# Kernel tuning notes

Hardware: AMD Instinct MI355X
Metric: run time of the kernel (lower is better)

## Reference

```python
import jax, jax.numpy as jnp
import numpy as np

OBS_X, OBS_Y, RADIUS = 40.0, 15.0, 6.0
B = 524288  # batch of states


def setup_inputs() -> dict:
    key = jax.random.key(0)
    ks = jax.random.split(key, 14)
    def lin_w(k, o, i):
        return jax.random.normal(k, (o, i), jnp.float32) * (1.0 / np.sqrt(i))
    return {
        "x": jax.random.normal(ks[0], (B, 5), jnp.float32),
        "sgn": 1,
        "mean": jax.random.normal(ks[1], (5,), jnp.float32),
        "std": jax.random.uniform(ks[2], (5,), jnp.float32, minval=0.5, maxval=1.5),
        "fc1_w": lin_w(ks[3], 128, 5),
        "fc1_b": jax.random.normal(ks[4], (128,), jnp.float32) * 0.1,
        "fc21_w": lin_w(ks[5], 32, 128),
        "fc21_b": jax.random.normal(ks[6], (32,), jnp.float32) * 0.1,
        "fc22_w": lin_w(ks[7], 32, 128),
        "fc22_b": jax.random.normal(ks[8], (32,), jnp.float32) * 0.1,
        "fc31_w": lin_w(ks[9], 2, 32),
        "fc31_b": jax.random.normal(ks[10], (2,), jnp.float32) * 0.1,
        "fc32_w": lin_w(ks[11], 2, 32),
        "fc32_b": jax.random.normal(ks[12], (2,), jnp.float32) * 0.1,
    }


def reference(x, sgn, mean, std, fc1_w, fc1_b, fc21_w, fc21_b,
              fc22_w, fc22_b, fc31_w, fc31_b, fc32_w, fc32_b):
    # --- tiny MLP (DynamicUnicycle2D config: 5 -> 128 -> {32,32} -> {2,2}) ---
    x0 = x * std + mean                                   # de-normalized state [B,5]
    h1 = jax.nn.relu(x @ fc1_w.T + fc1_b)                 # [B,128]
    x21 = jax.nn.relu(h1 @ fc21_w.T + fc21_b)             # [B,32]
    x22 = jax.nn.relu(h1 @ fc22_w.T + fc22_b)             # [B,32]
    x31 = x21 @ fc31_w.T + fc31_b                         # QP linear cost p, [B,2]
    x32 = 4.0 * jax.nn.sigmoid(x22 @ fc32_w.T + fc32_b)   # CBF class-K gains, [B,2]

    # --- CBF derivation (relative degree 2, circular obstacle) ---
    px, py, theta, v = x0[:, 0], x0[:, 1], x0[:, 2], x0[:, 3]
    s, c = jnp.sin(theta), jnp.cos(theta)
    dx, dy = px - OBS_X, py - OBS_Y
    barrier = dx * dx + dy * dy - RADIUS * RADIUS
    barrier_dot = 2.0 * dx * v * c + 2.0 * dy * v * s
    Lf2b = 2.0 * v * v
    LgLfbu1 = -2.0 * dx * v * s + 2.0 * dy * v * c
    LgLfbu2 = 2.0 * dx * c + 2.0 * dy * s
    G = jnp.stack([-LgLfbu1, -LgLfbu2], axis=1)           # [B,2], single row constraint
    h = Lf2b + (x32[:, 0] + x32[:, 1]) * barrier_dot + x32[:, 0] * x32[:, 1] * barrier  # [B]

    # --- batched QP: min 0.5 u^T u + p^T u  s.t.  G u <= h  (Q = I, one constraint)
    # Exact KKT solution: project unconstrained optimum onto the half-space.
    u0 = -x31                                             # unconstrained optimum
    viol = jnp.sum(G * u0, axis=1) - h                    # [B]
    gg = jnp.sum(G * G, axis=1)                           # [B]
    lam = jnp.maximum(viol, 0.0) / (gg + 1e-12)           # active-set multiplier
    u = u0 - lam[:, None] * G                             # [B,2] safe control
    return u
```

## Files before the change

kernel.cpp:

```cpp
#include <hip/hip_runtime.h>
#include <hip/hip_bf16.h>
#include <math.h>

typedef __attribute__((ext_vector_type(8))) _Float16 half8;
typedef __attribute__((ext_vector_type(4))) float f32x4;

#define OBS_X 40.0f
#define OBS_Y 15.0f
#define RADIUS 6.0f

__device__ __forceinline__ unsigned short f16hi(float v) {
    _Float16 h = (_Float16)v;
    return __builtin_bit_cast(unsigned short, h);
}
__device__ __forceinline__ float f16f(unsigned short b) {
    return (float)__builtin_bit_cast(_Float16, b);
}

__global__ void prep_kernel(const float* __restrict__ w1,
                            const float* __restrict__ w21,
                            const float* __restrict__ w22,
                            unsigned short* __restrict__ ws) {
    int tid = blockIdx.x * blockDim.x + threadIdx.x;
#pragma unroll
    for (int m = 0; m < 2; ++m) {
        int idx = tid * 2 + m;
        int j = idx & 7, l = (idx >> 3) & 63, kc = (idx >> 9) & 3, t = idx >> 11;
        int c = t * 16 + (l & 15);
        int k = kc * 32 + (l >> 4) * 8 + j;
        float v = (c < 32) ? w21[c * 128 + k] : w22[(c - 32) * 128 + k];
        _Float16 h  = (_Float16)v;
        _Float16 lo = (_Float16)(v - (float)h);
        ws[idx]        = __builtin_bit_cast(unsigned short, h);
        ws[8192 + idx] = __builtin_bit_cast(unsigned short, lo);
    }
    if (tid < 1024) {
        int j = tid & 7, fr = tid >> 3;
        float v = (j < 5) ? w1[fr * 5 + j] : 0.0f;
        _Float16 h  = (_Float16)v;
        _Float16 lo = (_Float16)(v - (float)h);
        ws[16384 + tid] = __builtin_bit_cast(unsigned short, h);
        ws[17408 + tid] = __builtin_bit_cast(unsigned short, lo);
    }
}

#define MFMA4(acc, ah_, al_, bh_, bl_)                                      \
    acc = __builtin_amdgcn_mfma_f32_16x16x32_f16(al_, bl_, acc, 0, 0, 0);   \
    acc = __builtin_amdgcn_mfma_f32_16x16x32_f16(al_, bh_, acc, 0, 0, 0);   \
    acc = __builtin_amdgcn_mfma_f32_16x16x32_f16(ah_, bl_, acc, 0, 0, 0);   \
    acc = __builtin_amdgcn_mfma_f32_16x16x32_f16(ah_, bh_, acc, 0, 0, 0);

__global__ __launch_bounds__(256, 4) void barriernet_mfma(
    const float* __restrict__ x,
    const float* __restrict__ mean_, const float* __restrict__ std_,
    const float* __restrict__ b1,
    const float* __restrict__ b21, const float* __restrict__ b22,
    const float* __restrict__ w31, const float* __restrict__ b31,
    const float* __restrict__ w32, const float* __restrict__ b32,
    const unsigned short* __restrict__ ws,
    float* __restrict__ out)
{
    __shared__ unsigned char smem[4 * 8192];
    const int tid  = threadIdx.x;
    const int lane = tid & 63;
    const int wv   = tid >> 6;
    const int r16  = lane & 15;
    const int g    = lane >> 4;
    unsigned char* h1hi = smem + wv * 8192;
    unsigned char* h1lo = h1hi + 4096;

    const int rowbase = blockIdx.x * 64 + wv * 16;
    const unsigned swz = ((unsigned)(r16 & 7)) << 4;

    float xv0 = 0.f, xv1 = 0.f, xv2 = 0.f, xv3 = 0.f;
    half8 bxh = {0,0,0,0,0,0,0,0}, bxl = {0,0,0,0,0,0,0,0};
    if (lane < 16) {
        const float* xr = x + (size_t)(rowbase + r16) * 5;
        float v4;
        xv0 = xr[0]; xv1 = xr[1]; xv2 = xr[2]; xv3 = xr[3]; v4 = xr[4];
        _Float16 h;
        h = (_Float16)xv0; bxh[0] = h; bxl[0] = (_Float16)(xv0 - (float)h);
        h = (_Float16)xv1; bxh[1] = h; bxl[1] = (_Float16)(xv1 - (float)h);
        h = (_Float16)xv2; bxh[2] = h; bxl[2] = (_Float16)(xv2 - (float)h);
        h = (_Float16)xv3; bxh[3] = h; bxl[3] = (_Float16)(xv3 - (float)h);
        h = (_Float16)v4;  bxh[4] = h; bxl[4] = (_Float16)(v4  - (float)h);
    }

#pragma unroll
    for (int t = 0; t < 8; ++t) {
        half8 awh = {0,0,0,0,0,0,0,0}, awl = {0,0,0,0,0,0,0,0};
        if (lane < 16) {
            awh = *(const half8*)(ws + 16384 + (t * 16 + lane) * 8);
            awl = *(const half8*)(ws + 17408 + (t * 16 + lane) * 8);
        }
        const float4 bb = *(const float4*)(b1 + t * 16 + g * 4);
        f32x4 acc = {bb.x, bb.y, bb.z, bb.w};
        MFMA4(acc, awh, awl, bxh, bxl);
        float v0 = fmaxf(acc[0], 0.f), v1 = fmaxf(acc[1], 0.f);
        float v2 = fmaxf(acc[2], 0.f), v3 = fmaxf(acc[3], 0.f);
        unsigned short h0 = f16hi(v0), h1v = f16hi(v1), h2 = f16hi(v2), h3 = f16hi(v3);
        unsigned short l0 = f16hi(v0 - f16f(h0)), l1 = f16hi(v1 - f16f(h1v));
        unsigned short l2 = f16hi(v2 - f16f(h2)), l3 = f16hi(v3 - f16f(h3));
        const unsigned off = ((unsigned)(32 * t + 8 * g)) ^ swz;
        uint2 ph; ph.x = (unsigned)h0 | ((unsigned)h1v << 16); ph.y = (unsigned)h2 | ((unsigned)h3 << 16);
        uint2 pl; pl.x = (unsigned)l0 | ((unsigned)l1  << 16); pl.y = (unsigned)l2 | ((unsigned)l3 << 16);
        *(uint2*)(h1hi + r16 * 256 + off) = ph;
        *(uint2*)(h1lo + r16 * 256 + off) = pl;
    }

    half8 ah[4], al[4];
#pragma unroll
    for (int kc = 0; kc < 4; ++kc) {
        const unsigned off = ((unsigned)(kc * 64 + g * 16)) ^ swz;
        ah[kc] = *(const half8*)(h1hi + r16 * 256 + off);
        al[kc] = *(const half8*)(h1lo + r16 * 256 + off);
    }
    f32x4 acc2[4];
#pragma unroll
    for (int t = 0; t < 4; ++t) {
        const float bias = (t < 2) ? b21[t * 16 + r16] : b22[(t - 2) * 16 + r16];
        f32x4 a = {bias, bias, bias, bias};
#pragma unroll
        for (int kc = 0; kc < 4; ++kc) {
            const half8 bh = *(const half8*)(ws + ((t * 4 + kc) * 64 + lane) * 8);
            const half8 bl = *(const half8*)(ws + 8192 + ((t * 4 + kc) * 64 + lane) * 8);
            MFMA4(a, ah[kc], al[kc], bh, bl);
        }
        acc2[t] = a;
    }

    const float w310a = w31[r16],      w310b = w31[16 + r16];
    const float w311a = w31[32 + r16], w311b = w31[48 + r16];
    const float w320a = w32[r16],      w320b = w32[16 + r16];
    const float w321a = w32[32 + r16], w321b = w32[48 + r16];
    float A0 = 0.f, A1 = 0.f, A2 = 0.f, A3 = 0.f;
    const int src = (lane >> 2) << 4;
#pragma unroll
    for (int r = 0; r < 4; ++r) {
        float v0 = fmaxf(acc2[0][r], 0.f), v1 = fmaxf(acc2[1][r], 0.f);
        float v2 = fmaxf(acc2[2][r], 0.f), v3 = fmaxf(acc2[3][r], 0.f);
        float p0 = v0 * w310a + v1 * w310b;
        float p1 = v0 * w311a + v1 * w311b;
        float p2 = v2 * w320a + v3 * w320b;
        float p3 = v2 * w321a + v3 * w321b;
#pragma unroll
        for (int d = 1; d <= 8; d <<= 1) {
            p0 += __shfl_xor(p0, d);
            p1 += __shfl_xor(p1, d);
            p2 += __shfl_xor(p2, d);
            p3 += __shfl_xor(p3, d);
        }
        float q0 = __shfl(p0, src), q1 = __shfl(p1, src);
        float q2 = __shfl(p2, src), q3 = __shfl(p3, src);
        if ((lane & 3) == r) { A0 = q0; A1 = q1; A2 = q2; A3 = q3; }
    }

    if (lane < 16) {
        const float a31_0 = A0 + b31[0], a31_1 = A1 + b31[1];
        const float a32_0 = A2 + b32[0], a32_1 = A3 + b32[1];
        const float s0 = 4.0f / (1.0f + __expf(-a32_0));
        const float s1 = 4.0f / (1.0f + __expf(-a32_1));
        const float px = fmaf(xv0, std_[0], mean_[0]);
        const float py = fmaf(xv1, std_[1], mean_[1]);
        const float th = fmaf(xv2, std_[2], mean_[2]);
        const float v  = fmaf(xv3, std_[3], mean_[3]);
        float sn, cs; __sincosf(th, &sn, &cs);
        const float dx = px - OBS_X, dy = py - OBS_Y;
        const float barrier     = dx * dx + dy * dy - RADIUS * RADIUS;
        const float barrier_dot = 2.f * dx * v * cs + 2.f * dy * v * sn;
        const float Lf2b = 2.f * v * v;
        const float G0 = 2.f * dx * v * sn - 2.f * dy * v * cs;
        const float G1 = -(2.f * dx * cs + 2.f * dy * sn);
        const float h  = Lf2b + (s0 + s1) * barrier_dot + s0 * s1 * barrier;
        const float u00 = -a31_0, u01 = -a31_1;
        const float viol = G0 * u00 + G1 * u01 - h;
        const float gg   = G0 * G0 + G1 * G1;
        const float lam  = fmaxf(viol, 0.f) / (gg + 1e-12f);
        float2 uo = make_float2(fmaf(-lam, G0, u00), fmaf(-lam, G1, u01));
        ((float2*)out)[rowbase + lane] = uo;
    }
}

extern "C" void kernel_launch(void* const* d_in, const int* in_sizes, int n_in,
                              void* d_out, int out_size, void* d_ws, size_t ws_size,
                              hipStream_t stream) {
    const float* x     = (const float*)d_in[0];
    const float* mean_ = (const float*)d_in[2];
    const float* std_  = (const float*)d_in[3];
    const float* w1    = (const float*)d_in[4];
    const float* b1    = (const float*)d_in[5];
    const float* w21   = (const float*)d_in[6];
    const float* b21   = (const float*)d_in[7];
    const float* w22   = (const float*)d_in[8];
    const float* b22   = (const float*)d_in[9];
    const float* w31   = (const float*)d_in[10];
    const float* b31   = (const float*)d_in[11];
    const float* w32   = (const float*)d_in[12];
    const float* b32   = (const float*)d_in[13];
    unsigned short* ws = (unsigned short*)d_ws;

    const int n = in_sizes[0] / 5;
    prep_kernel<<<16, 256, 0, stream>>>(w1, w21, w22, ws);
    barriernet_mfma<<<n / 64, 256, 0, stream>>>(
        x, mean_, std_, b1, b21, b22, w31, b31, w32, b32, ws, (float*)d_out);
}
```

Baseline: 154.5 us.

## Fuse weight prep into persistent MFMA kernel with register-resident layer-2 weights

Removes the separate weight-prep launch. Each block now splits w1 into hi/lo halves in LDS and keeps the layer-2 weights in registers as split fp16. Each wave processes 8 row tiles in a loop over a fixed 1024-block grid and prefetches the next tile's x. The change also drops the lo*lo MFMA term, folds b1 into the GEMM through a constant-1 input column, and simplifies the layer-3 reduction by swapping operand roles so results land per row. The aims are fewer launches, reuse of weight conversion across tiles, and fewer MFMAs and shuffles. In exchange it uses far more registers (launch bounds of 2) and the grid size is hardcoded to the batch.

```diff
diff --git a/kernel.cpp b/kernel.cpp
--- a/kernel.cpp
+++ b/kernel.cpp
@@ -3,64 +3,39 @@
 #include <math.h>
 
 typedef __attribute__((ext_vector_type(8))) _Float16 half8;
+typedef __attribute__((ext_vector_type(2))) _Float16 half2v;
 typedef __attribute__((ext_vector_type(4))) float f32x4;
 
 #define OBS_X 40.0f
 #define OBS_Y 15.0f
 #define RADIUS 6.0f
-
-__device__ __forceinline__ unsigned short f16hi(float v) {
-    _Float16 h = (_Float16)v;
-    return __builtin_bit_cast(unsigned short, h);
-}
-__device__ __forceinline__ float f16f(unsigned short b) {
-    return (float)__builtin_bit_cast(_Float16, b);
-}
-
-__global__ void prep_kernel(const float* __restrict__ w1,
-                            const float* __restrict__ w21,
-                            const float* __restrict__ w22,
-                            unsigned short* __restrict__ ws) {
-    int tid = blockIdx.x * blockDim.x + threadIdx.x;
-#pragma unroll
-    for (int m = 0; m < 2; ++m) {
-        int idx = tid * 2 + m;
-        int j = idx & 7, l = (idx >> 3) & 63, kc = (idx >> 9) & 3, t = idx >> 11;
-        int c = t * 16 + (l & 15);
-        int k = kc * 32 + (l >> 4) * 8 + j;
-        float v = (c < 32) ? w21[c * 128 + k] : w22[(c - 32) * 128 + k];
-        _Float16 h  = (_Float16)v;
-        _Float16 lo = (_Float16)(v - (float)h);
-        ws[idx]        = __builtin_bit_cast(unsigned short, h);
-        ws[8192 + idx] = __builtin_bit_cast(unsigned short, lo);
-    }
-    if (tid < 1024) {
-        int j = tid & 7, fr = tid >> 3;
-        float v = (j < 5) ? w1[fr * 5 + j] : 0.0f;
-        _Float16 h  = (_Float16)v;
-        _Float16 lo = (_Float16)(v - (float)h);
-        ws[16384 + tid] = __builtin_bit_cast(unsigned short, h);
-        ws[17408 + tid] = __builtin_bit_cast(unsigned short, lo);
-    }
-}
-
-#define MFMA4(acc, ah_, al_, bh_, bl_)                                      \
-    acc = __builtin_amdgcn_mfma_f32_16x16x32_f16(al_, bl_, acc, 0, 0, 0);   \
-    acc = __builtin_amdgcn_mfma_f32_16x16x32_f16(al_, bh_, acc, 0, 0, 0);   \
-    acc = __builtin_amdgcn_mfma_f32_16x16x32_f16(ah_, bl_, acc, 0, 0, 0);   \
-    acc = __builtin_amdgcn_mfma_f32_16x16x32_f16(ah_, bh_, acc, 0, 0, 0);
-
-__global__ __launch_bounds__(256, 4) void barriernet_mfma(
+#define TPW 8
+#define GRID 1024
+
+__device__ __forceinline__ half2v pkrtz(float a, float b) {
+    return __builtin_bit_cast(half2v, __builtin_amdgcn_cvt_pkrtz(a, b));
+}
+
+__device__ __forceinline__ void split8(const float* v, half8& hi, half8& lo) {
+#pragma unroll
+    for (int j = 0; j < 8; ++j) {
+        _Float16 h = (_Float16)v[j];
+        hi[j] = h;
+        lo[j] = (_Float16)(v[j] - (float)h);
+    }
+}
+
+__global__ __launch_bounds__(256, 2) void barriernet_fused(
     const float* __restrict__ x,
     const float* __restrict__ mean_, const float* __restrict__ std_,
-    const float* __restrict__ b1,
-    const float* __restrict__ b21, const float* __restrict__ b22,
+    const float* __restrict__ w1,  const float* __restrict__ b1,
+    const float* __restrict__ w21, const float* __restrict__ b21,
+    const float* __restrict__ w22, const float* __restrict__ b22,
     const float* __restrict__ w31, const float* __restrict__ b31,
     const float* __restrict__ w32, const float* __restrict__ b32,
-    const unsigned short* __restrict__ ws,
     float* __restrict__ out)
 {
-    __shared__ unsigned char smem[4 * 8192];
+    __shared__ unsigned char smem[36864];
     const int tid  = threadIdx.x;
     const int lane = tid & 63;
     const int wv   = tid >> 6;
@@ -68,116 +43,170 @@
     const int g    = lane >> 4;
     unsigned char* h1hi = smem + wv * 8192;
     unsigned char* h1lo = h1hi + 4096;
-
-    const int rowbase = blockIdx.x * 64 + wv * 16;
+    unsigned short* w1h_lds = (unsigned short*)(smem + 32768);
+    unsigned short* w1l_lds = w1h_lds + 1024;
     const unsigned swz = ((unsigned)(r16 & 7)) << 4;
-
-    float xv0 = 0.f, xv1 = 0.f, xv2 = 0.f, xv3 = 0.f;
+    const int slot = blockIdx.x * 4 + wv;
+
+    if (tid < 128) {
+        float v[8];
+#pragma unroll
+        for (int j = 0; j < 5; ++j) v[j] = w1[tid * 5 + j];
+        v[5] = b1[tid];
+        v[6] = 0.f; v[7] = 0.f;
+        half8 hi, lo;
+        split8(v, hi, lo);
+        *(half8*)(w1h_lds + tid * 8) = hi;
+        *(half8*)(w1l_lds + tid * 8) = lo;
+    }
+
+    half8 w2h[4][4], w2l[4][4];
+#pragma unroll
+    for (int t = 0; t < 4; ++t) {
+        const int r = 16 * t + r16;
+        const float* src = (r < 32) ? (w21 + r * 128) : (w22 + (r - 32) * 128);
+#pragma unroll
+        for (int kc = 0; kc < 4; ++kc) {
+            const float4 f0 = *(const float4*)(src + kc * 32 + g * 8);
+            const float4 f1 = *(const float4*)(src + kc * 32 + g * 8 + 4);
+            float v[8];
+            v[0] = f0.x; v[1] = f0.y; v[2] = f0.z; v[3] = f0.w;
+            v[4] = f1.x; v[5] = f1.y; v[6] = f1.z; v[7] = f1.w;
+            split8(v, w2h[t][kc], w2l[t][kc]);
+        }
+    }
+
+    __syncthreads();
+
+    const float m0 = mean_[0], m1 = mean_[1], m2 = mean_[2], m3 = mean_[3];
+    const float sd0 = std_[0], sd1 = std_[1], sd2 = std_[2], sd3 = std_[3];
+    const float bb31_0 = b31[0], bb31_1 = b31[1], bb32_0 = b32[0], bb32_1 = b32[1];
+
     half8 bxh = {0,0,0,0,0,0,0,0}, bxl = {0,0,0,0,0,0,0,0};
+    if (lane < 16) bxh[5] = (_Float16)1.0f;
+
+    float xa0 = 0.f, xa1 = 0.f, xa2 = 0.f, xa3 = 0.f, xa4 = 0.f;
     if (lane < 16) {
-        const float* xr = x + (size_t)(rowbase + r16) * 5;
-        float v4;
-        xv0 = xr[0]; xv1 = xr[1]; xv2 = xr[2]; xv3 = xr[3]; v4 = xr[4];
-        _Float16 h;
-        h = (_Float16)xv0; bxh[0] = h; bxl[0] = (_Float16)(xv0 - (float)h);
-        h = (_Float16)xv1; bxh[1] = h; bxl[1] = (_Float16)(xv1 - (float)h);
-        h = (_Float16)xv2; bxh[2] = h; bxl[2] = (_Float16)(xv2 - (float)h);
-        h = (_Float16)xv3; bxh[3] = h; bxl[3] = (_Float16)(xv3 - (float)h);
-        h = (_Float16)v4;  bxh[4] = h; bxl[4] = (_Float16)(v4  - (float)h);
-    }
-
-#pragma unroll
-    for (int t = 0; t < 8; ++t) {
-        half8 awh = {0,0,0,0,0,0,0,0}, awl = {0,0,0,0,0,0,0,0};
+        const float* xr = x + (size_t)(slot * TPW * 16 + r16) * 5;
+        xa0 = xr[0]; xa1 = xr[1]; xa2 = xr[2]; xa3 = xr[3]; xa4 = xr[4];
+    }
+
+#pragma unroll 1
+    for (int it = 0; it < TPW; ++it) {
+        const int rowbase = (slot * TPW + it) * 16;
+
         if (lane < 16) {
-            awh = *(const half8*)(ws + 16384 + (t * 16 + lane) * 8);
-            awl = *(const half8*)(ws + 17408 + (t * 16 + lane) * 8);
-        }
-        const float4 bb = *(const float4*)(b1 + t * 16 + g * 4);
-        f32x4 acc = {bb.x, bb.y, bb.z, bb.w};
-        MFMA4(acc, awh, awl, bxh, bxl);
-        float v0 = fmaxf(acc[0], 0.f), v1 = fmaxf(acc[1], 0.f);
-        float v2 = fmaxf(acc[2], 0.f), v3 = fmaxf(acc[3], 0.f);
-        unsigned short h0 = f16hi(v0), h1v = f16hi(v1), h2 = f16hi(v2), h3 = f16hi(v3);
-        unsigned short l0 = f16hi(v0 - f16f(h0)), l1 = f16hi(v1 - f16f(h1v));
-        unsigned short l2 = f16hi(v2 - f16f(h2)), l3 = f16hi(v3 - f16f(h3));
-        const unsigned off = ((unsigned)(32 * t + 8 * g)) ^ swz;
-        uint2 ph; ph.x = (unsigned)h0 | ((unsigned)h1v << 16); ph.y = (unsigned)h2 | ((unsigned)h3 << 16);
-        uint2 pl; pl.x = (unsigned)l0 | ((unsigned)l1  << 16); pl.y = (unsigned)l2 | ((unsigned)l3 << 16);
-        *(uint2*)(h1hi + r16 * 256 + off) = ph;
-        *(uint2*)(h1lo + r16 * 256 + off) = pl;
-    }
-
-    half8 ah[4], al[4];
-#pragma unroll
-    for (int kc = 0; kc < 4; ++kc) {
-        const unsigned off = ((unsigned)(kc * 64 + g * 16)) ^ swz;
-        ah[kc] = *(const half8*)(h1hi + r16 * 256 + off);
-        al[kc] = *(const half8*)(h1lo + r16 * 256 + off);
-    }
-    f32x4 acc2[4];
-#pragma unroll
-    for (int t = 0; t < 4; ++t) {
-        const float bias = (t < 2) ? b21[t * 16 + r16] : b22[(t - 2) * 16 + r16];
-        f32x4 a = {bias, bias, bias, bias};
+            _Float16 h;
+            h = (_Float16)xa0; bxh[0] = h; bxl[0] = (_Float16)(xa0 - (float)h);
+            h = (_Float16)xa1; bxh[1] = h; bxl[1] = (_Float16)(xa1 - (float)h);
+            h = (_Float16)xa2; bxh[2] = h; bxl[2] = (_Float16)(xa2 - (float)h);
+            h = (_Float16)xa3; bxh[3] = h; bxl[3] = (_Float16)(xa3 - (float)h);
+            h = (_Float16)xa4; bxh[4] = h; bxl[4] = (_Float16)(xa4 - (float)h);
+        }
+        const float xc0 = xa0, xc1 = xa1, xc2 = xa2, xc3 = xa3;
+
+        if (it + 1 < TPW && lane < 16) {
+            const float* xr = x + (size_t)(rowbase + 16 + r16) * 5;
+            xa0 = xr[0]; xa1 = xr[1]; xa2 = xr[2]; xa3 = xr[3]; xa4 = xr[4];
+        }
+
+#pragma unroll
+        for (int t8 = 0; t8 < 8; ++t8) {
+            half8 awh = {0,0,0,0,0,0,0,0}, awl = {0,0,0,0,0,0,0,0};
+            if (lane < 16) {
+                awh = *(const half8*)(w1h_lds + (t8 * 16 + r16) * 8);
+                awl = *(const half8*)(w1l_lds + (t8 * 16 + r16) * 8);
+            }
+            f32x4 acc = {0.f, 0.f, 0.f, 0.f};
+            acc = __builtin_amdgcn_mfma_f32_16x16x32_f16(awh, bxl, acc, 0, 0, 0);
+            acc = __builtin_amdgcn_mfma_f32_16x16x32_f16(awl, bxh, acc, 0, 0, 0);
+            acc = __builtin_amdgcn_mfma_f32_16x16x32_f16(awh, bxh, acc, 0, 0, 0);
+            float v0 = fmaxf(acc[0], 0.f), v1 = fmaxf(acc[1], 0.f);
+            float v2 = fmaxf(acc[2], 0.f), v3 = fmaxf(acc[3], 0.f);
+            half2v hA = pkrtz(v0, v1);
+            half2v hB = pkrtz(v2, v3);
+            half2v lA = pkrtz(v0 - (float)hA[0], v1 - (float)hA[1]);
+            half2v lB = pkrtz(v2 - (float)hB[0], v3 - (float)hB[1]);
+            const unsigned off = ((unsigned)(32 * t8 + 8 * g)) ^ swz;
+            uint2 ph; ph.x = __builtin_bit_cast(unsigned, hA); ph.y = __builtin_bit_cast(unsigned, hB);
+            uint2 pl; pl.x = __builtin_bit_cast(unsigned, lA); pl.y = __builtin_bit_cast(unsigned, lB);
+            *(uint2*)(h1hi + r16 * 256 + off) = ph;
+            *(uint2*)(h1lo + r16 * 256 + off) = pl;
+        }
+
+        asm volatile("" ::: "memory");
+
+        half8 ah[4], al[4];
 #pragma unroll
         for (int kc = 0; kc < 4; ++kc) {
-            const half8 bh = *(const half8*)(ws + ((t * 4 + kc) * 64 + lane) * 8);
-            const half8 bl = *(const half8*)(ws + 8192 + ((t * 4 + kc) * 64 + lane) * 8);
-            MFMA4(a, ah[kc], al[kc], bh, bl);
-        }
-        acc2[t] = a;
-    }
-
-    const float w310a = w31[r16],      w310b = w31[16 + r16];
-    const float w311a = w31[32 + r16], w311b = w31[48 + r16];
-    const float w320a = w32[r16],      w320b = w32[16 + r16];
-    const float w321a = w32[32 + r16], w321b = w32[48 + r16];
-    float A0 = 0.f, A1 = 0.f, A2 = 0.f, A3 = 0.f;
-    const int src = (lane >> 2) << 4;
-#pragma unroll
-    for (int r = 0; r < 4; ++r) {
-        float v0 = fmaxf(acc2[0][r], 0.f), v1 = fmaxf(acc2[1][r], 0.f);
-        float v2 = fmaxf(acc2[2][r], 0.f), v3 = fmaxf(acc2[3][r], 0.f);
-        float p0 = v0 * w310a + v1 * w310b;
-        float p1 = v0 * w311a + v1 * w311b;
-        float p2 = v2 * w320a + v3 * w320b;
-        float p3 = v2 * w321a + v3 * w321b;
-#pragma unroll
-        for (int d = 1; d <= 8; d <<= 1) {
-            p0 += __shfl_xor(p0, d);
-            p1 += __shfl_xor(p1, d);
-            p2 += __shfl_xor(p2, d);
-            p3 += __shfl_xor(p3, d);
-        }
-        float q0 = __shfl(p0, src), q1 = __shfl(p1, src);
-        float q2 = __shfl(p2, src), q3 = __shfl(p3, src);
-        if ((lane & 3) == r) { A0 = q0; A1 = q1; A2 = q2; A3 = q3; }
-    }
-
-    if (lane < 16) {
-        const float a31_0 = A0 + b31[0], a31_1 = A1 + b31[1];
-        const float a32_0 = A2 + b32[0], a32_1 = A3 + b32[1];
-        const float s0 = 4.0f / (1.0f + __expf(-a32_0));
-        const float s1 = 4.0f / (1.0f + __expf(-a32_1));
-        const float px = fmaf(xv0, std_[0], mean_[0]);
-        const float py = fmaf(xv1, std_[1], mean_[1]);
-        const float th = fmaf(xv2, std_[2], mean_[2]);
-        const float v  = fmaf(xv3, std_[3], mean_[3]);
-        float sn, cs; __sincosf(th, &sn, &cs);
-        const float dx = px - OBS_X, dy = py - OBS_Y;
-        const float barrier     = dx * dx + dy * dy - RADIUS * RADIUS;
-        const float barrier_dot = 2.f * dx * v * cs + 2.f * dy * v * sn;
-        const float Lf2b = 2.f * v * v;
-        const float G0 = 2.f * dx * v * sn - 2.f * dy * v * cs;
-        const float G1 = -(2.f * dx * cs + 2.f * dy * sn);
-        const float h  = Lf2b + (s0 + s1) * barrier_dot + s0 * s1 * barrier;
-        const float u00 = -a31_0, u01 = -a31_1;
-        const float viol = G0 * u00 + G1 * u01 - h;
-        const float gg   = G0 * G0 + G1 * G1;
-        const float lam  = fmaxf(viol, 0.f) / (gg + 1e-12f);
-        float2 uo = make_float2(fmaf(-lam, G0, u00), fmaf(-lam, G1, u01));
-        ((float2*)out)[rowbase + lane] = uo;
+            const unsigned off = ((unsigned)(kc * 64 + g * 16)) ^ swz;
+            ah[kc] = *(const half8*)(h1hi + r16 * 256 + off);
+            al[kc] = *(const half8*)(h1lo + r16 * 256 + off);
+        }
+        f32x4 acc2[4];
+#pragma unroll
+        for (int t = 0; t < 4; ++t) {
+            const float4 bb2 = (t < 2) ? *(const float4*)(b21 + 16 * t + 4 * g)
+                                       : *(const float4*)(b22 + 16 * (t - 2) + 4 * g);
+            f32x4 a = {bb2.x, bb2.y, bb2.z, bb2.w};
+#pragma unroll
+            for (int kc = 0; kc < 4; ++kc) {
+                a = __builtin_amdgcn_mfma_f32_16x16x32_f16(w2h[t][kc], al[kc], a, 0, 0, 0);
+                a = __builtin_amdgcn_mfma_f32_16x16x32_f16(w2l[t][kc], ah[kc], a, 0, 0, 0);
+                a = __builtin_amdgcn_mfma_f32_16x16x32_f16(w2h[t][kc], ah[kc], a, 0, 0, 0);
+            }
+            acc2[t] = a;
+        }
+
+        asm volatile("" ::: "memory");
+
+        const f32x4 wA0 = *(const f32x4*)(w31 + 4 * g);
+        const f32x4 wA1 = *(const f32x4*)(w31 + 16 + 4 * g);
+        const f32x4 wB0 = *(const f32x4*)(w31 + 32 + 4 * g);
+        const f32x4 wB1 = *(const f32x4*)(w31 + 48 + 4 * g);
+        const f32x4 wC0 = *(const f32x4*)(w32 + 4 * g);
+        const f32x4 wC1 = *(const f32x4*)(w32 + 16 + 4 * g);
+        const f32x4 wD0 = *(const f32x4*)(w32 + 32 + 4 * g);
+        const f32x4 wD1 = *(const f32x4*)(w32 + 48 + 4 * g);
+        float p0 = 0.f, p1 = 0.f, p2 = 0.f, p3 = 0.f;
+#pragma unroll
+        for (int r = 0; r < 4; ++r) {
+            float v0 = fmaxf(acc2[0][r], 0.f), v1 = fmaxf(acc2[1][r], 0.f);
+            float v2 = fmaxf(acc2[2][r], 0.f), v3 = fmaxf(acc2[3][r], 0.f);
+            p0 += wA0[r] * v0 + wA1[r] * v1;
+            p1 += wB0[r] * v0 + wB1[r] * v1;
+            p2 += wC0[r] * v2 + wC1[r] * v3;
+            p3 += wD0[r] * v2 + wD1[r] * v3;
+        }
+        p0 += __shfl_xor(p0, 16); p0 += __shfl_xor(p0, 32);
+        p1 += __shfl_xor(p1, 16); p1 += __shfl_xor(p1, 32);
+        p2 += __shfl_xor(p2, 16); p2 += __shfl_xor(p2, 32);
+        p3 += __shfl_xor(p3, 16); p3 += __shfl_xor(p3, 32);
+
+        if (lane < 16) {
+            const float a31_0 = p0 + bb31_0, a31_1 = p1 + bb31_1;
+            const float a32_0 = p2 + bb32_0, a32_1 = p3 + bb32_1;
+            const float s0 = 4.0f / (1.0f + __expf(-a32_0));
+            const float s1 = 4.0f / (1.0f + __expf(-a32_1));
+            const float px = fmaf(xc0, sd0, m0);
+            const float py = fmaf(xc1, sd1, m1);
+            const float th = fmaf(xc2, sd2, m2);
+            const float v  = fmaf(xc3, sd3, m3);
+            float sn, cs; __sincosf(th, &sn, &cs);
+            const float dx = px - OBS_X, dy = py - OBS_Y;
+            const float barrier     = dx * dx + dy * dy - RADIUS * RADIUS;
+            const float barrier_dot = 2.f * dx * v * cs + 2.f * dy * v * sn;
+            const float Lf2b = 2.f * v * v;
+            const float G0 = 2.f * dx * v * sn - 2.f * dy * v * cs;
+            const float G1 = -(2.f * dx * cs + 2.f * dy * sn);
+            const float h  = Lf2b + (s0 + s1) * barrier_dot + s0 * s1 * barrier;
+            const float u00 = -a31_0, u01 = -a31_1;
+            const float viol = G0 * u00 + G1 * u01 - h;
+            const float gg   = G0 * G0 + G1 * G1;
+            const float lam  = fmaxf(viol, 0.f) / (gg + 1e-12f);
+            float2 uo = make_float2(fmaf(-lam, G0, u00), fmaf(-lam, G1, u01));
+            ((float2*)out)[rowbase + r16] = uo;
+        }
     }
 }
 
@@ -197,10 +226,8 @@
     const float* b31   = (const float*)d_in[11];
     const float* w32   = (const float*)d_in[12];
     const float* b32   = (const float*)d_in[13];
-    unsigned short* ws = (unsigned short*)d_ws;
-
-    const int n = in_sizes[0] / 5;
-    prep_kernel<<<16, 256, 0, stream>>>(w1, w21, w22, ws);
-    barriernet_mfma<<<n / 64, 256, 0, stream>>>(
-        x, mean_, std_, b1, b21, b22, w31, b31, w32, b32, ws, (float*)d_out);
-}
+
+    barriernet_fused<<<GRID, 256, 0, stream>>>(
+        x, mean_, std_, w1, b1, w21, b21, w22, b22, w31, b31, w32, b32,
+        (float*)d_out);
+}
```

Result: faster. 146.1 us (-5.4%).
